# Performance work log

Hardware: AMD Instinct MI355X
Metric: run time of the kernel (lower is better)

## Reference

```python
import jax, jax.numpy as jnp
import numpy as np

LOCAL_SIZE = 128
LN_EPS = 1e-5


def _ln(x):
    # F.layer_norm over last axis, no affine params
    mu = jnp.mean(x, axis=-1, keepdims=True)
    var = jnp.var(x, axis=-1, keepdims=True)
    return (x - mu) / jnp.sqrt(var + LN_EPS)


def _rel_shift(x):
    # x: [b, n, qlen, klen] -> Transformer-XL relative shift
    b, n, q, k = x.shape
    xp = jnp.pad(x, ((0, 0), (0, 0), (0, 0), (1, 0)))
    xp = xp.reshape(b, n, k + 1, q)
    return xp[:, :, 1:, :].reshape(b, n, q, k)


def setup_inputs() -> dict:
    key = jax.random.key(0)
    ks = jax.random.split(key, 12)
    bsz, d_model, qlen, mlen = 16, 1024, 256, 256
    n_head, d_head, d_inner = 16, 64, 4096
    klen = qlen + mlen
    s = 0.02  # param init scale
    return {
        "z1ss": jax.random.normal(ks[0], (bsz, d_model, qlen), jnp.float32),
        "uss": jax.random.normal(ks[1], (bsz, 3 * n_head * d_head, klen), jnp.float32) * 0.1,
        "mems": jax.random.normal(ks[2], (bsz, d_model, mlen), jnp.float32),
        "pos_emb": jax.random.normal(ks[3], (d_model, klen), jnp.float32),
        "Wqkv": jax.random.normal(ks[4], (3 * n_head * d_head, d_model), jnp.float32) * s,
        "Wr": jax.random.normal(ks[5], (n_head * d_head, d_model), jnp.float32) * s,
        "Wo": jax.random.normal(ks[6], (d_model, n_head * d_head), jnp.float32) * s,
        "bo": jnp.zeros((d_model,), jnp.float32),
        "r_w_bias": jax.random.uniform(ks[7], (n_head, d_head), jnp.float32, -0.05, 0.05),
        "r_r_bias": jax.random.uniform(ks[8], (n_head, d_head), jnp.float32, -0.05, 0.05),
        "W1": jax.random.normal(ks[9], (d_inner, d_model), jnp.float32) * s,
        "b1": jnp.zeros((d_inner,), jnp.float32),
        "W2": jax.random.normal(ks[10], (d_model, d_inner), jnp.float32) * s,
        "b2": jnp.zeros((d_model,), jnp.float32),
    }


def reference(z1ss, uss, mems, pos_emb, Wqkv, Wr, Wo, bo, r_w_bias, r_r_bias, W1, b1, W2, b2):
    bsz, d_model, qlen = z1ss.shape
    mlen = mems.shape[-1]
    n_head, d_head = r_w_bias.shape
    scale = 1.0 / (d_head ** 0.5)

    # ---- self-attention with relative positions ----
    cat = jnp.concatenate([mems, z1ss], axis=-1)            # [b, d, klen]
    klen = cat.shape[-1]
    w_heads = jnp.einsum('od,bdk->bok', Wqkv, cat) + uss     # [b, 3*n*dh, klen]
    r_head_k = (Wr @ pos_emb).reshape(n_head, d_head, -1)    # [n, dh, rlen]

    q, k, v = jnp.split(w_heads, 3, axis=1)
    q = q[:, :, -qlen:].reshape(bsz, n_head, d_head, qlen)   # [b, n, dh, q]
    k = k.reshape(bsz, n_head, d_head, klen)
    v = v.reshape(bsz, n_head, d_head, klen)

    AC = jnp.einsum('bndi,bndj->bnij', q + r_w_bias[:, :, None], k)
    BD = jnp.einsum('bndi,ndj->bnij', q + r_r_bias[:, :, None], r_head_k)
    BD = _rel_shift(BD)
    attn_score = (AC + BD) * scale                            # [b, n, q, klen]

    # causal + local-window mask
    i = jnp.arange(qlen)[:, None]
    j = jnp.arange(klen)[None, :]
    mask = (j > i + mlen) | (j <= i + mlen - LOCAL_SIZE)      # [q, klen]
    attn_score = jnp.where(mask[None, None], -1e30, attn_score)

    attn_prob = jax.nn.softmax(attn_score, axis=-1)
    attn_vec = jnp.einsum('bnij,bndj->bndi', attn_prob, v)    # [b, n, dh, q]
    attn_vec = attn_vec.reshape(bsz, n_head * d_head, qlen)
    attn_out = jnp.einsum('od,bdq->boq', Wo, attn_vec) + bo[None, :, None]

    # post-LN residual (pre_lnorm=False), work in [b, q, d]
    h = _ln((attn_out + z1ss).transpose(0, 2, 1))             # [b, q, d]

    # ---- position-wise FF ----
    ff = jax.nn.relu(jnp.einsum('bqd,id->bqi', h, W1) + b1)
    ff = jnp.einsum('bqi,di->bqd', ff, W2) + b2
    out = _ln(ff + h)                                          # [b, q, d]
    return out.transpose(0, 2, 1)                              # [b, d, q]
```

## Files before the change

### kernel.cpp

```cpp
#include <hip/hip_runtime.h>
#include <hip/hip_bf16.h>
#include <math.h>

#define BSZ    16
#define DMODEL 1024
#define QLEN   256
#define MLEN   256
#define KLEN   512
#define NHEAD  16
#define DHEAD  64
#define DINNER 4096

typedef __bf16 bf16;
typedef bf16 bf16x8 __attribute__((ext_vector_type(8)));
typedef float f32x4 __attribute__((ext_vector_type(4)));

#define GLOBAL_AS __attribute__((address_space(1)))
#define LDS_AS    __attribute__((address_space(3)))

__global__ __launch_bounds__(256) void prep_k(
    const float* __restrict__ Wqkv, const float* __restrict__ Wr,
    const float* __restrict__ Wo,   const float* __restrict__ W1,
    const float* __restrict__ W2,   const float* __restrict__ uss,
    const float* __restrict__ mems, const float* __restrict__ z1ss,
    const float* __restrict__ pos_emb,
    bf16* __restrict__ WqkvB, bf16* __restrict__ WrB, bf16* __restrict__ WoB,
    bf16* __restrict__ W1B,   bf16* __restrict__ W2B, bf16* __restrict__ ussV,
    bf16* __restrict__ catT,  bf16* __restrict__ posT,
    bf16* __restrict__ ussQ,  bf16* __restrict__ ussK)
{
    if (blockIdx.x < 21504) {
        long long i = (long long)blockIdx.x * 256 + threadIdx.x;
        const float* src; bf16* dst; long long soff, doff;
        if      (i <  786432) { src = Wqkv; dst = WqkvB; soff = doff = i; }
        else if (i < 1048576) { src = Wr;   dst = WrB;   soff = doff = i -  786432; }
        else if (i < 1310720) { src = Wo;   dst = WoB;   soff = doff = i - 1048576; }
        else if (i < 2359296) { src = W1;   dst = W1B;   soff = doff = i - 1310720; }
        else if (i < 3407872) { src = W2;   dst = W2B;   soff = doff = i - 2359296; }
        else {
            long long u = i - 3407872, b = u >> 17, r = u & 131071;
            src = uss; dst = ussV; soff = b * 393216 + 262144 + r; doff = u;
        }
        float4 v = ((const float4*)src)[soff];
        bf16 b0 = (bf16)v.x, b1 = (bf16)v.y, b2 = (bf16)v.z, b3 = (bf16)v.w;
        union { ushort u[4]; uint2 d; } p;
        p.u[0] = *(ushort*)&b0; p.u[1] = *(ushort*)&b1;
        p.u[2] = *(ushort*)&b2; p.u[3] = *(ushort*)&b3;
        ((uint2*)dst)[doff] = p.d;
        return;
    }
    __shared__ float tile[32][33];
    int blk = blockIdx.x - 21504;
    const float* src; bf16* dst; long long soff, dof; int ld, ldo, tr, tc;
    if (blk < 8192) {
        int bh = blk >> 8, t = blk & 255;
        int b = bh >> 1, half = bh & 1;
        tr = t >> 3; tc = t & 7;
        src = half ? z1ss : mems; soff = (long long)b * 1024 * 256; ld = 256;
        dst = catT; dof = ((long long)b * 512 + half * 256) * 1024; ldo = 1024;
    } else if (blk < 8704) {
        int u = blk - 8192; tr = u >> 4; tc = u & 15;
        src = pos_emb; soff = 0; ld = 512;
        dst = posT; dof = 0; ldo = 1024;
    } else if (blk < 12800) {
        int u = blk - 8704; int b = u >> 8, t = u & 255;
        tr = t >> 3; tc = t & 7;
        src = uss; soff = (long long)b * 3072 * 512 + 256; ld = 512;
        dst = ussQ; dof = (long long)b * 256 * 1024; ldo = 1024;
    } else {
        int u = blk - 12800; int b = u >> 9, t = u & 511;
        tr = t >> 4; tc = t & 15;
        src = uss; soff = ((long long)b * 3072 + 1024) * 512; ld = 512;
        dst = ussK; dof = (long long)b * 512 * 1024; ldo = 1024;
    }
    int tx = threadIdx.x & 31, ty = threadIdx.x >> 5;
    const float* ip = src + soff;
#pragma unroll
    for (int yy = ty; yy < 32; yy += 8)
        tile[yy][tx] = ip[(long long)(tr * 32 + yy) * ld + tc * 32 + tx];
    __syncthreads();
#pragma unroll
    for (int yy = ty; yy < 32; yy += 8)
        dst[dof + (long long)(tc * 32 + yy) * ldo + tr * 32 + tx] = (bf16)tile[tx][yy];
}

__global__ __launch_bounds__(256) void qkv_gemm_k(
    const bf16* __restrict__ catT, const bf16* __restrict__ WqkvB,
    const bf16* __restrict__ posT, const bf16* __restrict__ WrB,
    const bf16* __restrict__ ussQ, const bf16* __restrict__ ussK,
    const bf16* __restrict__ ussV,
    bf16* __restrict__ qT, bf16* __restrict__ kT,
    bf16* __restrict__ rhkT, bf16* __restrict__ vB)
{
    __shared__ bf16 lA[2 * 128 * 32];
    __shared__ bf16 lB[2 * 128 * 32];

    int id = blockIdx.x;
    int t = threadIdx.x;
    int w = t >> 6, lane = t & 63;

    const bf16 *Ap, *Bp;
    int mode, bz = 0, m0, n0;
    if (id < 768) {
        bz = id / 48; int r = id % 48;
        if (r < 32) { m0 = 256 + ((r >> 4) << 7); n0 = (r & 15) << 7; }
        else        { int rr = r - 32; m0 = (rr >> 3) << 7; n0 = (8 + (rr & 7)) << 7; }
        Ap = catT + (long long)bz * 512 * 1024; Bp = WqkvB; mode = 0;
    } else if (id < 800) {
        int rr = id - 768; m0 = (rr >> 3) << 7; n0 = (rr & 7) << 7;
        Ap = posT; Bp = WrB; mode = 1;
    } else {
        int rr = id - 800; bz = rr >> 5; int tt = rr & 31;
        m0 = (tt >> 2) << 7; n0 = (tt & 3) << 7;
        Ap = WqkvB + 2048 * 1024; Bp = catT + (long long)bz * 512 * 1024; mode = 2;
    }

    int q = lane >> 4, r16 = lane & 15;
    int wm = w >> 1, wn = w & 1;

    f32x4 acc[4][4];
#pragma unroll
    for (int i = 0; i < 4; ++i)
#pragma unroll
        for (int j = 0; j < 4; ++j)
            acc[i][j] = (f32x4){0.f, 0.f, 0.f, 0.f};

    int srow = lane >> 2;
    int scol = (lane & 3) * 8;

    for (int k0 = 0; k0 < 1024; k0 += 64) {
        __syncthreads();
#pragma unroll
        for (int half = 0; half < 2; ++half) {
#pragma unroll
            for (int issue = 0; issue < 2; ++issue) {
                int c = issue * 4 + w;
                int row = c * 16 + srow;
                int col = k0 + half * 32 + scol;
                __builtin_amdgcn_global_load_lds(
                    (const GLOBAL_AS void*)(Ap + (long long)(m0 + row) * 1024 + col),
                    (LDS_AS void*)(lA + half * 4096 + c * 512 + lane * 8), 16, 0, 0);
                __builtin_amdgcn_global_load_lds(
                    (const GLOBAL_AS void*)(Bp + (long long)(n0 + row) * 1024 + col),
                    (LDS_AS void*)(lB + half * 4096 + c * 512 + lane * 8), 16, 0, 0);
            }
        }
        __syncthreads();
#pragma unroll
        for (int kh = 0; kh < 2; ++kh) {
            bf16x8 af[4], bfr[4];
#pragma unroll
            for (int i = 0; i < 4; ++i)
                af[i] = *(const bf16x8*)&lA[kh * 4096 + (wm * 64 + i * 16 + r16) * 32 + q * 8];
#pragma unroll
            for (int j = 0; j < 4; ++j)
                bfr[j] = *(const bf16x8*)&lB[kh * 4096 + (wn * 64 + j * 16 + r16) * 32 + q * 8];
#pragma unroll
            for (int i = 0; i < 4; ++i)
#pragma unroll
                for (int j = 0; j < 4; ++j)
                    acc[i][j] = __builtin_amdgcn_mfma_f32_16x16x32_bf16(
                        af[i], bfr[j], acc[i][j], 0, 0, 0);
        }
    }

    bool isq = (mode == 0) && (n0 < 1024);
#pragma unroll
    for (int i = 0; i < 4; ++i) {
#pragma unroll
        for (int r = 0; r < 4; ++r) {
            int m = m0 + wm * 64 + i * 16 + q * 4 + r;
#pragma unroll
            for (int j = 0; j < 4; ++j) {
                int n = n0 + wn * 64 + j * 16 + r16;
                float v = acc[i][j][r];
                if (mode == 1) {
                    rhkT[(long long)m * 1024 + n] = (bf16)v;
                } else if (mode == 2) {
                    long long idx = ((long long)bz * 1024 + m) * 512 + n;
                    vB[idx] = (bf16)(v + (float)ussV[idx]);
                } else if (isq) {
                    long long idx = ((long long)(bz * 256 + m - 256) << 10) + n;
                    qT[idx] = (bf16)(v + (float)ussQ[idx]);
                } else {
                    long long idx = ((long long)(bz * 512 + m) << 10) + (n - 1024);
                    kT[idx] = (bf16)(v + (float)ussK[idx]);
                }
            }
        }
    }
}

__global__ __launch_bounds__(256) void gemm_bf16(
    const bf16* __restrict__ A, const bf16* __restrict__ B,
    int M, int N, int K, int kChunk,
    const float* __restrict__ bias, int relu,
    float* __restrict__ outF, long long ofBatch,
    bf16* __restrict__ outB)
{
    __shared__ bf16 lA[2 * 128 * 32];
    __shared__ bf16 lB[2 * 128 * 32];

    int t = threadIdx.x;
    int w = t >> 6, lane = t & 63;
    int m0 = blockIdx.y * 128, n0 = blockIdx.x * 128;
    int bz = blockIdx.z;

    const bf16* Ap = A;
    const bf16* Bp = B;
    float* oF = outF;
    int Keff = K;
    if (kChunk > 0) {
        Ap = A + (long long)bz * kChunk;
        Bp = B + (long long)bz * kChunk;
        if (outF) oF = outF + (long long)bz * ofBatch;
        Keff = kChunk;
    }

    int q = lane >> 4, r16 = lane & 15;
    int wm = w >> 1, wn = w & 1;

    f32x4 acc[4][4];
#pragma unroll
    for (int i = 0; i < 4; ++i)
#pragma unroll
        for (int j = 0; j < 4; ++j)
            acc[i][j] = (f32x4){0.f, 0.f, 0.f, 0.f};

    int srow = lane >> 2;
    int scol = (lane & 3) * 8;

    for (int k0 = 0; k0 < Keff; k0 += 64) {
        __syncthreads();
#pragma unroll
        for (int half = 0; half < 2; ++half) {
#pragma unroll
            for (int issue = 0; issue < 2; ++issue) {
                int c = issue * 4 + w;
                int row = c * 16 + srow;
                int col = k0 + half * 32 + scol;
                __builtin_amdgcn_global_load_lds(
                    (const GLOBAL_AS void*)(Ap + (long long)(m0 + row) * K + col),
                    (LDS_AS void*)(lA + half * 4096 + c * 512 + lane * 8), 16, 0, 0);
                __builtin_amdgcn_global_load_lds(
                    (const GLOBAL_AS void*)(Bp + (long long)(n0 + row) * K + col),
                    (LDS_AS void*)(lB + half * 4096 + c * 512 + lane * 8), 16, 0, 0);
            }
        }
        __syncthreads();
#pragma unroll
        for (int kh = 0; kh < 2; ++kh) {
            bf16x8 af[4], bfr[4];
#pragma unroll
            for (int i = 0; i < 4; ++i)
                af[i] = *(const bf16x8*)&lA[kh * 4096 + (wm * 64 + i * 16 + r16) * 32 + q * 8];
#pragma unroll
            for (int j = 0; j < 4; ++j)
                bfr[j] = *(const bf16x8*)&lB[kh * 4096 + (wn * 64 + j * 16 + r16) * 32 + q * 8];
#pragma unroll
            for (int i = 0; i < 4; ++i)
#pragma unroll
                for (int j = 0; j < 4; ++j)
                    acc[i][j] = __builtin_amdgcn_mfma_f32_16x16x32_bf16(
                        af[i], bfr[j], acc[i][j], 0, 0, 0);
        }
    }

#pragma unroll
    for (int i = 0; i < 4; ++i) {
#pragma unroll
        for (int r = 0; r < 4; ++r) {
            int m = m0 + wm * 64 + i * 16 + q * 4 + r;
#pragma unroll
            for (int j = 0; j < 4; ++j) {
                int n = n0 + wn * 64 + j * 16 + r16;
                float v = acc[i][j][r];
                if (bias) v += bias[n];
                if (relu) v = fmaxf(v, 0.f);
                if (oF)   oF[(long long)m * N + n] = v;
                if (outB) outB[(long long)m * N + n] = (bf16)v;
            }
        }
    }
}

__global__ __launch_bounds__(256) void attn_mfma_k(
    const bf16* __restrict__ qT,
    const bf16* __restrict__ kT,
    const bf16* __restrict__ vB,
    const bf16* __restrict__ rhkT,
    const float* __restrict__ rwb,
    const float* __restrict__ rrb,
    bf16* __restrict__ avT)
{
    __shared__ float sBD[64][132];

    int t = threadIdx.x;
    int w = t >> 6, lane = t & 63;
    int lo = lane & 15, hi = lane >> 4;
    int i0 = blockIdx.x * 64;
    int n  = blockIdx.y;
    int b  = blockIdx.z;

    const bf16* qp = qT + ((long long)(b * 256 + i0 + 16 * w + lo)) * 1024 + n * 64;
    bf16x8 qw[2], qr[2];
#pragma unroll
    for (int ks = 0; ks < 2; ++ks) {
        bf16x8 qv = *(const bf16x8*)(qp + ks * 32 + hi * 8);
        const float* wb = rwb + n * 64 + ks * 32 + hi * 8;
        const float* rb = rrb + n * 64 + ks * 32 + hi * 8;
#pragma unroll
        for (int e = 0; e < 8; ++e) {
            float qf = (float)qv[e];
            qw[ks][e] = (bf16)(qf + wb[e]);
            qr[ks][e] = (bf16)(qf + rb[e]);
        }
    }

    const bf16* rp = rhkT + (long long)384 * 1024 + n * 64;
#pragma unroll
    for (int tj = 0; tj < 8; ++tj) {
        const bf16* bp = rp + (long long)(16 * tj + lo) * 1024;
        f32x4 a = (f32x4){0.f, 0.f, 0.f, 0.f};
        a = __builtin_amdgcn_mfma_f32_16x16x32_bf16(qr[0], *(const bf16x8*)(bp + hi * 8), a, 0, 0, 0);
        a = __builtin_amdgcn_mfma_f32_16x16x32_bf16(qr[1], *(const bf16x8*)(bp + 32 + hi * 8), a, 0, 0, 0);
#pragma unroll
        for (int r = 0; r < 4; ++r)
            sBD[16 * w + hi * 4 + r][16 * tj + lo] = a[r];
    }
    __syncthreads();

    f32x4 ac[12];
    const bf16* kp = kT + ((long long)b * 512 + i0 + 129) * 1024 + n * 64;
#pragma unroll
    for (int tj = 0; tj < 12; ++tj) {
        const bf16* bp = kp + (long long)(16 * tj + lo) * 1024;
        f32x4 a = (f32x4){0.f, 0.f, 0.f, 0.f};
        a = __builtin_amdgcn_mfma_f32_16x16x32_bf16(qw[0], *(const bf16x8*)(bp + hi * 8), a, 0, 0, 0);
        a = __builtin_amdgcn_mfma_f32_16x16x32_bf16(qw[1], *(const bf16x8*)(bp + 32 + hi * 8), a, 0, 0, 0);
        ac[tj] = a;
    }

    float p[12][4], rowmax[4], rowsum[4];
#pragma unroll
    for (int r = 0; r < 4; ++r) rowmax[r] = -1e30f;
#pragma unroll
    for (int tj = 0; tj < 12; ++tj) {
#pragma unroll
        for (int r = 0; r < 4; ++r) {
            int m = 16 * w + hi * 4 + r;
            int jj = 16 * tj + lo;
            int tt = jj - m;
            float v = (tt >= 0 && tt < 128) ? (ac[tj][r] + sBD[m][tt]) * 0.125f
                                            : -1e30f;
            p[tj][r] = v;
            rowmax[r] = fmaxf(rowmax[r], v);
        }
    }
#pragma unroll
    for (int r = 0; r < 4; ++r) {
        float mx = rowmax[r];
#pragma unroll
        for (int msk = 1; msk < 16; msk <<= 1)
            mx = fmaxf(mx, __shfl_xor(mx, msk, 64));
        rowmax[r] = mx;
        rowsum[r] = 0.f;
    }
#pragma unroll
    for (int tj = 0; tj < 12; ++tj) {
#pragma unroll
        for (int r = 0; r < 4; ++r) {
            float e = exp2f((p[tj][r] - rowmax[r]) * 1.44269504f);
            p[tj][r] = e;
            rowsum[r] += e;
        }
    }
#pragma unroll
    for (int r = 0; r < 4; ++r) {
        float s = rowsum[r];
#pragma unroll
        for (int msk = 1; msk < 16; msk <<= 1)
            s += __shfl_xor(s, msk, 64);
        rowsum[r] = 1.f / s;
    }

    bf16* P = (bf16*)&sBD[0][0];
#pragma unroll
    for (int tj = 0; tj < 12; ++tj) {
#pragma unroll
        for (int r = 0; r < 4; ++r) {
            int m = 16 * w + hi * 4 + r;
            P[m * 264 + 16 * tj + lo] = (bf16)(p[tj][r] * rowsum[r]);
        }
    }
    __syncthreads();

    f32x4 oacc[4];
#pragma unroll
    for (int td = 0; td < 4; ++td) oacc[td] = (f32x4){0.f, 0.f, 0.f, 0.f};
    const bf16* vp = vB + ((long long)b * 1024 + n * 64) * 512 + i0 + 129;
#pragma unroll
    for (int ks = 0; ks < 6; ++ks) {
        bf16x8 af = *(const bf16x8*)(P + (16 * w + lo) * 264 + ks * 32 + hi * 8);
#pragma unroll
        for (int td = 0; td < 4; ++td) {
            bf16x8 bv = *(const bf16x8*)(vp + (long long)(16 * td + lo) * 512 + ks * 32 + hi * 8);
            oacc[td] = __builtin_amdgcn_mfma_f32_16x16x32_bf16(af, bv, oacc[td], 0, 0, 0);
        }
    }
    bf16* op = avT + ((long long)(b * 256 + i0 + 16 * w)) * 1024 + n * 64;
#pragma unroll
    for (int td = 0; td < 4; ++td)
#pragma unroll
        for (int r = 0; r < 4; ++r)
            op[(long long)(hi * 4 + r) * 1024 + 16 * td + lo] = (bf16)oacc[td][r];
}

__global__ __launch_bounds__(256) void ln_bf16_k(
    const float* __restrict__ X1a, const float* __restrict__ X1b,
    const float* __restrict__ bo,  const bf16* __restrict__ catT,
    bf16* __restrict__ H)
{
    int row = blockIdx.x, t = threadIdx.x;
    __shared__ float r1[256], r2[256];
    const float* xa = X1a + (long long)row * 1024;
    const float* xb = X1b + (long long)row * 1024;
    const bf16*  zr = catT + ((long long)(row >> 8) * 512 + 256 + (row & 255)) * 1024;
    float v[4], s = 0.f, ss = 0.f;
#pragma unroll
    for (int u = 0; u < 4; ++u) {
        int c = t + u * 256;
        v[u] = xa[c] + xb[c] + bo[c] + (float)zr[c];
        s += v[u]; ss += v[u] * v[u];
    }
    r1[t] = s; r2[t] = ss;
    __syncthreads();
    for (int off = 128; off > 0; off >>= 1) {
        if (t < off) { r1[t] += r1[t + off]; r2[t] += r2[t + off]; }
        __syncthreads();
    }
    float mean = r1[0] * (1.f / 1024.f);
    float var  = r2[0] * (1.f / 1024.f) - mean * mean;
    float rstd = rsqrtf(var + 1e-5f);
    bf16* hr = H + (long long)row * 1024;
#pragma unroll
    for (int u = 0; u < 4; ++u)
        hr[t + u * 256] = (bf16)((v[u] - mean) * rstd);
}

__global__ __launch_bounds__(256) void ln_final_k(
    const bf16* __restrict__ Hb,
    const float* __restrict__ X2a, const float* __restrict__ X2b,
    const float* __restrict__ b2,
    float* __restrict__ O)
{
    int row = blockIdx.x, t = threadIdx.x;
    int b = row >> 8, qq = row & 255;
    __shared__ float r1[256], r2[256];
    const float* xa = X2a + (long long)row * 1024;
    const float* xb = X2b + (long long)row * 1024;
    const bf16*  hr = Hb  + (long long)row * 1024;

    float y[4], s = 0.f, ss = 0.f;
#pragma unroll
    for (int u = 0; u < 4; ++u) {
        int c = t + u * 256;
        y[u] = xa[c] + xb[c] + b2[c] + (float)hr[c];
        s += y[u]; ss += y[u] * y[u];
    }
    r1[t] = s; r2[t] = ss;
    __syncthreads();
    for (int off = 128; off > 0; off >>= 1) {
        if (t < off) { r1[t] += r1[t + off]; r2[t] += r2[t + off]; }
        __syncthreads();
    }
    float mean = r1[0] * (1.f / 1024.f);
    float var  = r2[0] * (1.f / 1024.f) - mean * mean;
    float rstd = rsqrtf(var + 1e-5f);

    float* ob = O + (long long)b * 1024 * 256 + qq;
#pragma unroll
    for (int u = 0; u < 4; ++u)
        ob[(long long)(t + u * 256) * 256] = (y[u] - mean) * rstd;
}

extern "C" void kernel_launch(void* const* d_in, const int* in_sizes, int n_in,
                              void* d_out, int out_size, void* d_ws, size_t ws_size,
                              hipStream_t stream) {
    const float* z1ss    = (const float*)d_in[0];
    const float* uss     = (const float*)d_in[1];
    const float* mems    = (const float*)d_in[2];
    const float* pos_emb = (const float*)d_in[3];
    const float* Wqkv    = (const float*)d_in[4];
    const float* Wr      = (const float*)d_in[5];
    const float* Wo      = (const float*)d_in[6];
    const float* bo      = (const float*)d_in[7];
    const float* rwb     = (const float*)d_in[8];
    const float* rrb     = (const float*)d_in[9];
    const float* W1      = (const float*)d_in[10];
    const float* b1      = (const float*)d_in[11];
    const float* W2      = (const float*)d_in[12];
    const float* b2      = (const float*)d_in[13];

    char* base = (char*)d_ws;
    bf16*  catT  = (bf16*) (base + 0);
    bf16*  posT  = (bf16*) (base + 16777216);
    bf16*  WqkvB = (bf16*) (base + 17825792);
    bf16*  WrB   = (bf16*) (base + 24117248);
    bf16*  WoB   = (bf16*) (base + 26214400);
    bf16*  W1B   = (bf16*) (base + 28311552);
    bf16*  W2B   = (bf16*) (base + 36700160);
    bf16*  qTB   = (bf16*) (base + 45088768);
    bf16*  kTB   = (bf16*) (base + 53477376);
    bf16*  vBB   = (bf16*) (base + 70254592);
    float* x1a   = (float*)(base + 53477376);
    float* x1b   = (float*)(base + 70254592);
    bf16*  ff_b  = (bf16*) (base + 53477376);
    bf16*  rhkTB = (bf16*) (base + 87031808);
    bf16*  avTB  = (bf16*) (base + 88080384);
    bf16*  ussQb = (bf16*) (base + 96468992);
    bf16*  ussKb = (bf16*) (base + 104857600);
    bf16*  ussVb = (bf16*) (base + 121634816);
    float* x2a   = (float*)(base + 96468992);
    float* x2b   = (float*)(base + 113246208);
    bf16*  hB    = (bf16*) (base + 130023424);

    prep_k<<<42496, 256, 0, stream>>>(
        Wqkv, Wr, Wo, W1, W2, uss, mems, z1ss, pos_emb,
        WqkvB, WrB, WoB, W1B, W2B, ussVb, catT, posT, ussQb, ussKb);

    qkv_gemm_k<<<1312, 256, 0, stream>>>(
        catT, WqkvB, posT, WrB, ussQb, ussKb, ussVb, qTB, kTB, rhkTB, vBB);

    attn_mfma_k<<<dim3(4, NHEAD, BSZ), 256, 0, stream>>>(
        qTB, kTB, vBB, rhkTB, rwb, rrb, avTB);

    gemm_bf16<<<dim3(8, 32, 2), 256, 0, stream>>>(
        avTB, WoB, 4096, 1024, 1024, 512,
        nullptr, 0, x1a, (long long)(x1b - x1a), nullptr);

    ln_bf16_k<<<4096, 256, 0, stream>>>(x1a, x1b, bo, catT, hB);

    gemm_bf16<<<dim3(32, 32, 1), 256, 0, stream>>>(
        hB, W1B, 4096, 4096, 1024, 0,
        b1, 1, nullptr, 0, ff_b);

    gemm_bf16<<<dim3(8, 32, 2), 256, 0, stream>>>(
        ff_b, W2B, 4096, 1024, 4096, 2048,
        nullptr, 0, x2a, (long long)(x2b - x2a), nullptr);

    ln_final_k<<<4096, 256, 0, stream>>>(hB, x2a, x2b, b2, (float*)d_out);
}
```

Before: 594.8 us.

## Use 256x256 8-wave pipelined GEMM core for QKV and FF1 projections

Replaces the 128x128 4-wave QKV GEMM and the FF1 GEMM with a new 512-thread kernel using 256x256 tiles. It double-buffers K-slices in LDS with async global-to-LDS loads interleaved across four MFMA phases, uses XOR-swizzled LDS layouts to avoid bank conflicts, and remaps block IDs across the XCDs. The larger tiles cut global traffic per FLOP and aim to hide load latency behind MFMAs. In exchange each block uses 128KB of LDS and many accumulator registers, which limits occupancy, and the QKV grid drops to 328 blocks, which may leave CUs unevenly loaded.

```diff
diff --git a/kernel.cpp b/kernel.cpp
--- a/kernel.cpp
+++ b/kernel.cpp
@@ -84,7 +84,121 @@
         dst[dof + (long long)(tc * 32 + yy) * ldo + tr * 32 + tx] = (bf16)tile[tx][yy];
 }
 
-__global__ __launch_bounds__(256) void qkv_gemm_k(
+
+__device__ __forceinline__ void stage_a_unit(const bf16* __restrict__ Ag, int ldK,
+                                             bf16* sAbuf, int qa, int t) {
+    int r  = (t >> 2) & 63;
+    int ks = t >> 8;
+    int cc = (t & 3) ^ (((t >> 5) & 1) << 1);
+    int col = ks * 32 + cc * 8;
+    __builtin_amdgcn_global_load_lds(
+        (const GLOBAL_AS void*)(Ag + (long long)(qa * 64 + r) * ldK + col),
+        (LDS_AS void*)(sAbuf + qa * 4096 + t * 8), 16, 0, 0);
+    __builtin_amdgcn_global_load_lds(
+        (const GLOBAL_AS void*)(Ag + (long long)(qa * 64 + 128 + r) * ldK + col),
+        (LDS_AS void*)(sAbuf + (qa + 2) * 4096 + t * 8), 16, 0, 0);
+}
+
+__device__ __forceinline__ void stage_b_unit(const bf16* __restrict__ Bg, int ldK,
+                                             bf16* sBbuf, int qb, int t) {
+#pragma unroll
+    for (int j = 0; j < 2; ++j) {
+        int u  = j * 512 + t;
+        int p  = u >> 8;
+        int w8 = u & 255;
+        int ks = w8 >> 7;
+        int r  = (w8 >> 2) & 31;
+        int cc = (u & 3) ^ (((t >> 5) & 1) << 1);
+        __builtin_amdgcn_global_load_lds(
+            (const GLOBAL_AS void*)(Bg + (long long)(p * 64 + qb * 32 + r) * ldK + ks * 32 + cc * 8),
+            (LDS_AS void*)(sBbuf + p * 4096 + ks * 2048 + qb * 1024 + r * 32 + (u & 3) * 8),
+            16, 0, 0);
+    }
+}
+
+__device__ __forceinline__ void ld_a(const bf16* sAbuf, int qa, int wm, int lane,
+                                     bf16x8 a[4][2]) {
+    int r16 = lane & 15, qq = lane >> 4;
+    int flip = ((r16 >> 3) & 1) << 4;
+    const bf16* base = sAbuf + (wm * 2 + qa) * 4096;
+#pragma unroll
+    for (int mf = 0; mf < 4; ++mf)
+#pragma unroll
+        for (int ks = 0; ks < 2; ++ks)
+            a[mf][ks] = *(const bf16x8*)(base +
+                ((ks * 2048 + (mf * 16 + r16) * 32 + qq * 8) ^ flip));
+}
+
+__device__ __forceinline__ void ld_b(const bf16* sBbuf, int qb, int wn, int lane,
+                                     bf16x8 b[2][2]) {
+    int r16 = lane & 15, qq = lane >> 4;
+    int flip = ((r16 >> 3) & 1) << 4;
+    const bf16* base = sBbuf + wn * 4096 + qb * 1024;
+#pragma unroll
+    for (int nf = 0; nf < 2; ++nf)
+#pragma unroll
+        for (int ks = 0; ks < 2; ++ks)
+            b[nf][ks] = *(const bf16x8*)(base +
+                ((ks * 2048 + (nf * 16 + r16) * 32 + qq * 8) ^ flip));
+}
+
+#define PH_SYNC_MFMA(QA, QB)                                                   \
+    __builtin_amdgcn_s_barrier();                                              \
+    asm volatile("s_waitcnt lgkmcnt(0)" ::: "memory");                         \
+    __builtin_amdgcn_s_setprio(1);                                             \
+    _Pragma("unroll") for (int ks = 0; ks < 2; ++ks)                           \
+    _Pragma("unroll") for (int mf = 0; mf < 4; ++mf)                           \
+    _Pragma("unroll") for (int nf = 0; nf < 2; ++nf)                           \
+        acc[(QA)*4+mf][(QB)*2+nf] = __builtin_amdgcn_mfma_f32_16x16x32_bf16(   \
+            a[mf][ks], b[nf][ks], acc[(QA)*4+mf][(QB)*2+nf], 0, 0, 0);         \
+    __builtin_amdgcn_s_setprio(0);                                             \
+    __builtin_amdgcn_s_barrier();
+
+__device__ __forceinline__ void gemm8_core(
+    const bf16* __restrict__ Ap, const bf16* __restrict__ Bp,
+    int ldK, int NT, bf16* sA, bf16* sB, f32x4 (&acc)[8][4])
+{
+    int t = threadIdx.x;
+    int lane = t & 63, w = t >> 6;
+    int wm = w >> 2, wn = w & 3;
+
+    stage_a_unit(Ap, ldK, sA, 0, t);
+    stage_a_unit(Ap, ldK, sA, 1, t);
+    stage_b_unit(Bp, ldK, sB, 0, t);
+    stage_b_unit(Bp, ldK, sB, 1, t);
+    stage_b_unit(Bp + 64, ldK, sB + 16384, 0, t);
+    stage_a_unit(Ap + 64, ldK, sA + 16384, 1, t);
+    stage_b_unit(Bp + 64, ldK, sB + 16384, 1, t);
+    asm volatile("s_waitcnt vmcnt(6)" ::: "memory");
+    __builtin_amdgcn_s_barrier();
+
+    bf16x8 a[4][2], b[2][2];
+    for (int g = 0; g < NT; ++g) {
+        bf16* AR = sA + (g & 1) * 16384;
+        bf16* BR = sB + (g & 1) * 16384;
+        bf16* AO = sA + ((g & 1) ^ 1) * 16384;
+        const bf16* An = Ap + (long long)(g + 1) * 64;
+        const bf16* A2 = Ap + (long long)(g + 2) * 64;
+        const bf16* B2 = Bp + (long long)(g + 2) * 64;
+        ld_a(AR, 0, wm, lane, a);
+        ld_b(BR, 0, wn, lane, b);
+        if (g + 1 < NT) stage_a_unit(An, ldK, AO, 0, t);
+        PH_SYNC_MFMA(0, 0)
+        ld_a(AR, 1, wm, lane, a);
+        if (g + 2 < NT) stage_b_unit(B2, ldK, BR, 0, t);
+        PH_SYNC_MFMA(1, 0)
+        ld_b(BR, 1, wn, lane, b);
+        if (g + 2 < NT) stage_a_unit(A2, ldK, AR, 1, t);
+        PH_SYNC_MFMA(1, 1)
+        ld_a(AR, 0, wm, lane, a);
+        if (g + 2 < NT) stage_b_unit(B2, ldK, BR, 1, t);
+        if (g < NT - 2) asm volatile("s_waitcnt vmcnt(6)" ::: "memory");
+        else            asm volatile("s_waitcnt vmcnt(0)" ::: "memory");
+        PH_SYNC_MFMA(0, 1)
+    }
+}
+
+__global__ __launch_bounds__(512) void qkv8_k(
     const bf16* __restrict__ catT, const bf16* __restrict__ WqkvB,
     const bf16* __restrict__ posT, const bf16* __restrict__ WrB,
     const bf16* __restrict__ ussQ, const bf16* __restrict__ ussK,
@@ -92,100 +206,106 @@
     bf16* __restrict__ qT, bf16* __restrict__ kT,
     bf16* __restrict__ rhkT, bf16* __restrict__ vB)
 {
-    __shared__ bf16 lA[2 * 128 * 32];
-    __shared__ bf16 lB[2 * 128 * 32];
-
-    int id = blockIdx.x;
-    int t = threadIdx.x;
-    int w = t >> 6, lane = t & 63;
+    __shared__ bf16 sm[65536];
+    int f = blockIdx.x;
+    int id = (f & 7) * 41 + (f >> 3);
 
     const bf16 *Ap, *Bp;
-    int mode, bz = 0, m0, n0;
-    if (id < 768) {
-        bz = id / 48; int r = id % 48;
-        if (r < 32) { m0 = 256 + ((r >> 4) << 7); n0 = (r & 15) << 7; }
-        else        { int rr = r - 32; m0 = (rr >> 3) << 7; n0 = (8 + (rr & 7)) << 7; }
-        Ap = catT + (long long)bz * 512 * 1024; Bp = WqkvB; mode = 0;
-    } else if (id < 800) {
-        int rr = id - 768; m0 = (rr >> 3) << 7; n0 = (rr & 7) << 7;
-        Ap = posT; Bp = WrB; mode = 1;
+    bf16* outp; const bf16* addp;
+    long long obase; int ostr;
+    if (id < 320) {
+        int b = id / 20, rb = id % 20;
+        const bf16* cat = catT + (long long)b * 524288;
+        if (rb < 4) {
+            int n0 = rb << 8;
+            Ap = cat + 256 * 1024; Bp = WqkvB + (long long)n0 * 1024;
+            outp = qT; addp = ussQ;
+            obase = ((long long)b * 256) * 1024 + n0; ostr = 1024;
+        } else if (rb < 12) {
+            int rr = rb - 4, m0 = (rr >> 2) << 8, n0 = (rr & 3) << 8;
+            Ap = cat + (long long)m0 * 1024; Bp = WqkvB + (long long)(1024 + n0) * 1024;
+            outp = kT; addp = ussK;
+            obase = ((long long)(b * 512 + m0)) * 1024 + n0; ostr = 1024;
+        } else {
+            int rr = rb - 12, m0 = (rr >> 1) << 8, n0 = (rr & 1) << 8;
+            Ap = WqkvB + (long long)(2048 + m0) * 1024; Bp = cat + (long long)n0 * 1024;
+            outp = vB; addp = ussV;
+            obase = ((long long)(b * 1024 + m0)) * 512 + n0; ostr = 512;
+        }
     } else {
-        int rr = id - 800; bz = rr >> 5; int tt = rr & 31;
-        m0 = (tt >> 2) << 7; n0 = (tt & 3) << 7;
-        Ap = WqkvB + 2048 * 1024; Bp = catT + (long long)bz * 512 * 1024; mode = 2;
-    }
-
-    int q = lane >> 4, r16 = lane & 15;
-    int wm = w >> 1, wn = w & 1;
-
-    f32x4 acc[4][4];
-#pragma unroll
-    for (int i = 0; i < 4; ++i)
-#pragma unroll
-        for (int j = 0; j < 4; ++j)
-            acc[i][j] = (f32x4){0.f, 0.f, 0.f, 0.f};
-
-    int srow = lane >> 2;
-    int scol = (lane & 3) * 8;
-
-    for (int k0 = 0; k0 < 1024; k0 += 64) {
-        __syncthreads();
-#pragma unroll
-        for (int half = 0; half < 2; ++half) {
-#pragma unroll
-            for (int issue = 0; issue < 2; ++issue) {
-                int c = issue * 4 + w;
-                int row = c * 16 + srow;
-                int col = k0 + half * 32 + scol;
-                __builtin_amdgcn_global_load_lds(
-                    (const GLOBAL_AS void*)(Ap + (long long)(m0 + row) * 1024 + col),
-                    (LDS_AS void*)(lA + half * 4096 + c * 512 + lane * 8), 16, 0, 0);
-                __builtin_amdgcn_global_load_lds(
-                    (const GLOBAL_AS void*)(Bp + (long long)(n0 + row) * 1024 + col),
-                    (LDS_AS void*)(lB + half * 4096 + c * 512 + lane * 8), 16, 0, 0);
+        int r = id - 320, m0 = (r >> 2) << 8, n0 = (r & 3) << 8;
+        Ap = posT + (long long)m0 * 1024; Bp = WrB + (long long)n0 * 1024;
+        outp = rhkT; addp = nullptr;
+        obase = (long long)m0 * 1024 + n0; ostr = 1024;
+    }
+
+    f32x4 acc[8][4];
+#pragma unroll
+    for (int i = 0; i < 8; ++i)
+#pragma unroll
+        for (int j = 0; j < 4; ++j) acc[i][j] = (f32x4){0.f, 0.f, 0.f, 0.f};
+
+    gemm8_core(Ap, Bp, 1024, 16, sm, sm + 32768, acc);
+
+    int t = threadIdx.x, lane = t & 63, w = t >> 6;
+    int wm = w >> 2, wn = w & 3;
+    int qq = lane >> 4, r16 = lane & 15;
+#pragma unroll
+    for (int mf = 0; mf < 8; ++mf) {
+#pragma unroll
+        for (int rr2 = 0; rr2 < 4; ++rr2) {
+            int ml = wm * 128 + mf * 16 + qq * 4 + rr2;
+#pragma unroll
+            for (int nf = 0; nf < 4; ++nf) {
+                int nl = wn * 64 + nf * 16 + r16;
+                long long idx = obase + (long long)ml * ostr + nl;
+                float v = acc[mf][nf][rr2];
+                if (addp) v += (float)addp[idx];
+                outp[idx] = (bf16)v;
             }
         }
-        __syncthreads();
-#pragma unroll
-        for (int kh = 0; kh < 2; ++kh) {
-            bf16x8 af[4], bfr[4];
-#pragma unroll
-            for (int i = 0; i < 4; ++i)
-                af[i] = *(const bf16x8*)&lA[kh * 4096 + (wm * 64 + i * 16 + r16) * 32 + q * 8];
-#pragma unroll
-            for (int j = 0; j < 4; ++j)
-                bfr[j] = *(const bf16x8*)&lB[kh * 4096 + (wn * 64 + j * 16 + r16) * 32 + q * 8];
-#pragma unroll
-            for (int i = 0; i < 4; ++i)
-#pragma unroll
-                for (int j = 0; j < 4; ++j)
-                    acc[i][j] = __builtin_amdgcn_mfma_f32_16x16x32_bf16(
-                        af[i], bfr[j], acc[i][j], 0, 0, 0);
-        }
-    }
-
-    bool isq = (mode == 0) && (n0 < 1024);
-#pragma unroll
-    for (int i = 0; i < 4; ++i) {
-#pragma unroll
-        for (int r = 0; r < 4; ++r) {
-            int m = m0 + wm * 64 + i * 16 + q * 4 + r;
-#pragma unroll
-            for (int j = 0; j < 4; ++j) {
-                int n = n0 + wn * 64 + j * 16 + r16;
-                float v = acc[i][j][r];
-                if (mode == 1) {
-                    rhkT[(long long)m * 1024 + n] = (bf16)v;
-                } else if (mode == 2) {
-                    long long idx = ((long long)bz * 1024 + m) * 512 + n;
-                    vB[idx] = (bf16)(v + (float)ussV[idx]);
-                } else if (isq) {
-                    long long idx = ((long long)(bz * 256 + m - 256) << 10) + n;
-                    qT[idx] = (bf16)(v + (float)ussQ[idx]);
-                } else {
-                    long long idx = ((long long)(bz * 512 + m) << 10) + (n - 1024);
-                    kT[idx] = (bf16)(v + (float)ussK[idx]);
-                }
+    }
+}
+
+__global__ __launch_bounds__(512) void gemm8_k(
+    const bf16* __restrict__ A, const bf16* __restrict__ B,
+    int N, int K,
+    const float* __restrict__ bias, int relu,
+    bf16* __restrict__ outB)
+{
+    __shared__ bf16 sm[65536];
+    int nwg = gridDim.x, f = blockIdx.x;
+    int xcd = f & 7, l = f >> 3;
+    int q8 = nwg >> 3, rm = nwg & 7;
+    int wg = (xcd < rm) ? (xcd * (q8 + 1) + l)
+                        : (rm * (q8 + 1) + (xcd - rm) * q8 + l);
+    int ntn = N >> 8;
+    int m0 = (wg / ntn) << 8, n0 = (wg % ntn) << 8;
+
+    f32x4 acc[8][4];
+#pragma unroll
+    for (int i = 0; i < 8; ++i)
+#pragma unroll
+        for (int j = 0; j < 4; ++j) acc[i][j] = (f32x4){0.f, 0.f, 0.f, 0.f};
+
+    gemm8_core(A + (long long)m0 * K, B + (long long)n0 * K, K, K >> 6,
+               sm, sm + 32768, acc);
+
+    int t = threadIdx.x, lane = t & 63, w = t >> 6;
+    int wm = w >> 2, wn = w & 3;
+    int qq = lane >> 4, r16 = lane & 15;
+#pragma unroll
+    for (int mf = 0; mf < 8; ++mf) {
+#pragma unroll
+        for (int rr2 = 0; rr2 < 4; ++rr2) {
+            int m = m0 + wm * 128 + mf * 16 + qq * 4 + rr2;
+#pragma unroll
+            for (int nf = 0; nf < 4; ++nf) {
+                int n = n0 + wn * 64 + nf * 16 + r16;
+                float v = acc[mf][nf][rr2];
+                if (bias) v += bias[n];
+                if (relu) v = fmaxf(v, 0.f);
+                outB[(long long)m * N + n] = (bf16)v;
             }
         }
     }
@@ -529,7 +649,7 @@
         Wqkv, Wr, Wo, W1, W2, uss, mems, z1ss, pos_emb,
         WqkvB, WrB, WoB, W1B, W2B, ussVb, catT, posT, ussQb, ussKb);
 
-    qkv_gemm_k<<<1312, 256, 0, stream>>>(
+    qkv8_k<<<328, 512, 0, stream>>>(
         catT, WqkvB, posT, WrB, ussQb, ussKb, ussVb, qTB, kTB, rhkTB, vBB);
 
     attn_mfma_k<<<dim3(4, NHEAD, BSZ), 256, 0, stream>>>(
@@ -541,9 +661,8 @@
 
     ln_bf16_k<<<4096, 256, 0, stream>>>(x1a, x1b, bo, catT, hB);
 
-    gemm_bf16<<<dim3(32, 32, 1), 256, 0, stream>>>(
-        hB, W1B, 4096, 4096, 1024, 0,
-        b1, 1, nullptr, 0, ff_b);
+    gemm8_k<<<256, 512, 0, stream>>>(
+        hB, W1B, 4096, 1024, b1, 1, ff_b);
 
     gemm_bf16<<<dim3(8, 32, 2), 256, 0, stream>>>(
         ff_b, W2B, 4096, 1024, 4096, 2048,
```

After: 588.6 us. No clear change (-1.0%).
